# Kernel optimization log

Measured on AMD Instinct MI355X. Metric: run time of the kernel, lower is better.

The kernel has to match this reference:

```python
import jax, jax.numpy as jnp
import numpy as np

B, T, H, I = 256, 1024, 512, 1


def _uniform(key, shape, bound):
    return jax.random.uniform(key, shape, jnp.float32, -bound, bound)


def setup_inputs() -> dict:
    key = jax.random.key(0)
    ks = jax.random.split(key, 11)
    s = 1.0 / np.sqrt(H)
    return {
        "input": jax.random.normal(ks[0], (B, T), jnp.float32),
        "W_ih1": _uniform(ks[1], (3 * H, I), s),
        "W_hh1": _uniform(ks[2], (3 * H, H), s),
        "b_ih1": _uniform(ks[3], (3 * H,), s),
        "b_hh1": _uniform(ks[4], (3 * H,), s),
        "W_ih2": _uniform(ks[5], (3 * H, H), s),
        "W_hh2": _uniform(ks[6], (3 * H, H), s),
        "b_ih2": _uniform(ks[7], (3 * H,), s),
        "b_hh2": _uniform(ks[8], (3 * H,), s),
        "W_out": _uniform(ks[9], (1, H), s),
        "b_out": _uniform(ks[10], (1,), s),
        "future": 0,
    }


def _gru_cell(x, h, W_ih, W_hh, b_ih, b_hh):
    # PyTorch nn.GRUCell: gates ordered (r, z, n)
    gi = x @ W_ih.T + b_ih          # [B, 3H]
    gh = h @ W_hh.T + b_hh          # [B, 3H]
    i_r, i_z, i_n = jnp.split(gi, 3, axis=-1)
    h_r, h_z, h_n = jnp.split(gh, 3, axis=-1)
    r = jax.nn.sigmoid(i_r + h_r)
    z = jax.nn.sigmoid(i_z + h_z)
    n = jnp.tanh(i_n + r * h_n)
    return (1.0 - z) * n + z * h


def _run(input, W_ih1, W_hh1, b_ih1, b_hh1, W_ih2, W_hh2, b_ih2, b_hh2, W_out, b_out, future):
    Bb = input.shape[0]
    h0 = jnp.zeros((Bb, H), input.dtype)

    def step(carry, x_t):  # x_t: [B]
        h1, h2 = carry
        h1 = _gru_cell(x_t[:, None], h1, W_ih1, W_hh1, b_ih1, b_hh1)
        h2 = _gru_cell(h1, h2, W_ih2, W_hh2, b_ih2, b_hh2)
        out = h2 @ W_out.T + b_out  # [B, 1]
        return (h1, h2), out[:, 0]

    (h1, h2), ys = jax.lax.scan(step, (h0, h0), input.T)  # ys: [T, B]
    outs = [ys.T]  # [B, T]
    out = ys[-1][:, None]
    for _ in range(future):
        (h1, h2), o = step((h1, h2), out[:, 0])
        out = o[:, None]
        outs.append(out)
    return jnp.concatenate(outs, axis=1) if future > 0 else outs[0]


def reference(input, W_ih1, W_hh1, b_ih1, b_hh1, W_ih2, W_hh2, b_ih2, b_hh2, W_out, b_out, future):
    return _run(input, W_ih1, W_hh1, b_ih1, b_hh1, W_ih2, W_hh2, b_ih2, b_hh2, W_out, b_out, future)
```

## Files before the change

### kernel.cpp

```cpp
#include <hip/hip_runtime.h>

#define NB 256
#define NT 512
#define TT 1024
#define HH 512
#define BATCH 256

using v8s   = __attribute__((ext_vector_type(8))) short;
using f32x4 = __attribute__((ext_vector_type(4))) float;

#define O_RZ2I 0
#define O_RZ2H 32768
#define O_NA   65536
#define O_RZ1  98304
#define O_NB   131072
#define O_WOUT 147456
#define O_ZERO 149504
#define LDS_BYTES 162064

#define SLOT_SH 524288

__device__ __forceinline__ float sigf(float v)   { return 1.f / (1.f + __expf(-v)); }
__device__ __forceinline__ float tanhf_(float v) { return 2.f / (1.f + __expf(-2.f * v)) - 1.f; }

__device__ __forceinline__ unsigned short bf16_rne(float f) {
    union { float f; unsigned u; } a; a.f = f;
    unsigned r = (a.u + 0x7fffu + ((a.u >> 16) & 1u)) >> 16;
    return (unsigned short)r;
}
__device__ __forceinline__ float bf16_f(unsigned short h) {
    union { unsigned u; float f; } a; a.u = ((unsigned)h) << 16; return a.f;
}
__device__ __forceinline__ f32x4 MF(v8s a, v8s b, f32x4 c) {
    return __builtin_amdgcn_mfma_f32_16x16x32_bf16(a, b, c, 0, 0, 0);
}

#define GST2(addr, val) \
    asm volatile("global_store_short %0, %1, off sc0 sc1" \
                 :: "v"(addr), "v"(val) : "memory");

__device__ __forceinline__ void gridbar(unsigned* barr, int bg, int tid,
                                        unsigned ep, bool fence) {
    asm volatile("s_waitcnt vmcnt(0)" ::: "memory");
    __syncthreads();
    if (tid == 0) {
        unsigned* cnt = barr + bg * 64;
        __hip_atomic_fetch_add(cnt, 1u, __ATOMIC_RELAXED, __HIP_MEMORY_SCOPE_AGENT);
        while (__hip_atomic_load(cnt, __ATOMIC_RELAXED, __HIP_MEMORY_SCOPE_AGENT) < ep * 64u)
            __builtin_amdgcn_s_sleep(1);
        if (fence)
            __builtin_amdgcn_fence(__ATOMIC_ACQUIRE, "agent");
    }
    __syncthreads();
}

__global__ __launch_bounds__(256) void k_transpose(const float* __restrict__ x,
                                                   float* __restrict__ xT) {
    __shared__ float tile[64][65];
    const int bt = blockIdx.x, bb = blockIdx.y;
    const int lt = threadIdx.x & 63, lb = threadIdx.x >> 6;
    #pragma unroll 4
    for (int i = 0; i < 16; ++i) {
        int row = lb + i * 4;
        tile[row][lt] = x[(size_t)(bb * 64 + row) * TT + bt * 64 + lt];
    }
    __syncthreads();
    #pragma unroll 4
    for (int i = 0; i < 16; ++i) {
        int row = lb + i * 4;
        xT[(size_t)(bt * 64 + row) * BATCH + bb * 64 + lt] = tile[lt][row];
    }
}

__global__ __launch_bounds__(NT, 1) void gru_mfma(
    const float* __restrict__ xT,
    const float* __restrict__ Wih1, const float* __restrict__ Whh1,
    const float* __restrict__ bih1, const float* __restrict__ bhh1,
    const float* __restrict__ Wih2, const float* __restrict__ Whh2,
    const float* __restrict__ bih2, const float* __restrict__ bhh2,
    const float* __restrict__ Wout, const float* __restrict__ bout,
    float* __restrict__ out,
    unsigned short* __restrict__ hws,
    unsigned* __restrict__ barr,
    int rmask, int invmask)
{
    extern __shared__ char lds_b[];
    const int tid = threadIdx.x, blk = blockIdx.x;
    const int bg = blk >> 6, ug = blk & 63;
    const int u0 = ug * 8;

    for (int i = tid; i < 16 * 512; i += NT) {
        int n = i >> 9, k = i & 511;
        int row = (n < 8) ? (u0 + n) : (HH + u0 + (n - 8));
        float f = Wih2[(size_t)row * HH + k];
        unsigned short hi = bf16_rne(f), lo = bf16_rne(f - bf16_f(hi));
        int s = k >> 5, g = (k >> 3) & 3, j = k & 7, ln = g * 16 + n;
        int base = O_RZ2I + s * 2048 + ln * 16 + j * 2;
        *(unsigned short*)(lds_b + base) = hi;
        *(unsigned short*)(lds_b + base + 1024) = lo;
    }
    for (int i = tid; i < 16 * 512; i += NT) {
        int n = i >> 9, k = i & 511;
        int row = (n < 8) ? (u0 + n) : (HH + u0 + (n - 8));
        float f = Whh2[(size_t)row * HH + k];
        unsigned short hi = bf16_rne(f), lo = bf16_rne(f - bf16_f(hi));
        int s = k >> 5, g = (k >> 3) & 3, j = k & 7, ln = g * 16 + n;
        int base = O_RZ2H + s * 2048 + ln * 16 + j * 2;
        *(unsigned short*)(lds_b + base) = hi;
        *(unsigned short*)(lds_b + base + 1024) = lo;
    }
    for (int i = tid; i < 16 * 512; i += NT) {
        int n = i >> 9, k = i & 511;
        float f = (n < 8) ? Wih2[(size_t)(2 * HH + u0 + n) * HH + k]
                          : Whh1[(size_t)(2 * HH + u0 + (n - 8)) * HH + k];
        unsigned short hi = bf16_rne(f), lo = bf16_rne(f - bf16_f(hi));
        int s = k >> 5, g = (k >> 3) & 3, j = k & 7, ln = g * 16 + n;
        int base = O_NA + s * 2048 + ln * 16 + j * 2;
        *(unsigned short*)(lds_b + base) = hi;
        *(unsigned short*)(lds_b + base + 1024) = lo;
    }
    for (int i = tid; i < 16 * 512; i += NT) {
        int n = i >> 9, k = i & 511;
        int row = (n < 8) ? (u0 + n) : (HH + u0 + (n - 8));
        float f = Whh1[(size_t)row * HH + k];
        unsigned short hi = bf16_rne(f), lo = bf16_rne(f - bf16_f(hi));
        int s = k >> 5, g = (k >> 3) & 3, j = k & 7, ln = g * 16 + n;
        int base = O_RZ1 + s * 2048 + ln * 16 + j * 2;
        *(unsigned short*)(lds_b + base) = hi;
        *(unsigned short*)(lds_b + base + 1024) = lo;
    }
    for (int i = tid; i < 8 * 512; i += NT) {
        int c = i >> 9, k = i & 511;
        float f = Whh2[(size_t)(2 * HH + u0 + c) * HH + k];
        unsigned short hi = bf16_rne(f), lo = bf16_rne(f - bf16_f(hi));
        int s = k >> 5, g = (k >> 3) & 3, j = k & 7;
        int base = O_NB + s * 1024 + (g * 8 + c) * 16 + j * 2;
        *(unsigned short*)(lds_b + base) = hi;
        *(unsigned short*)(lds_b + base + 512) = lo;
    }
    for (int k = tid; k < 512; k += NT) {
        float f = Wout[k];
        unsigned short hi = bf16_rne(f), lo = bf16_rne(f - bf16_f(hi));
        int s = k >> 5, g = (k >> 3) & 3, j = k & 7;
        int base = O_WOUT + s * 64 + g * 16 + j * 2;
        *(unsigned short*)(lds_b + base) = hi;
        *(unsigned short*)(lds_b + base + 1024) = lo;
    }
    if (tid < 4) ((unsigned*)(lds_b + O_ZERO))[tid] = 0;

    {
        const int rl = tid >> 3, uo = tid & 7;
        const int b = bg * 64 + rl, u = u0 + uo;
        unsigned short* s0 = hws;
        GST2(s0 + 262144 + (size_t)b * HH + u, 0u);
        GST2(s0 + 393216 + (size_t)b * HH + u, 0u);
        float x0 = xT[b];
        float r = sigf(x0 * Wih1[u] + bih1[u] + bhh1[u]);
        float z = sigf(x0 * Wih1[HH + u] + bih1[HH + u] + bhh1[HH + u]);
        float n = tanhf_(x0 * Wih1[2 * HH + u] + bih1[2 * HH + u] + r * bhh1[2 * HH + u]);
        float h = (1.f - z) * n;
        unsigned short hi = bf16_rne(h), lo = bf16_rne(h - bf16_f(hi));
        GST2(s0 + (size_t)b * HH + u, (unsigned)hi);
        GST2(s0 + 131072 + (size_t)b * HH + u, (unsigned)lo);
    }

    const int w = tid >> 6, lane = tid & 63;
    const int n16 = lane & 15, g4 = lane >> 4;
    const int rt = w & 3, kh = w >> 2;
    const int c = n16, cu = c & 7;
    const int u = u0 + cu;
    const int sbase = kh * 8;

    float b2rz = 0, wx1 = 0, b1rz = 0, bin2_ = 0, bhn2_ = 0, wxn1 = 0, bin1_ = 0, bhn1_ = 0;
    float hprev[4] = {0.f, 0.f, 0.f, 0.f};
    if (kh == 1) {
        b2rz = (c < 8) ? bih2[u] + bhh2[u] : bih2[HH + u] + bhh2[HH + u];
        wx1  = (c < 8) ? Wih1[u] : Wih1[HH + u];
        b1rz = (c < 8) ? bih1[u] + bhh1[u] : bih1[HH + u] + bhh1[HH + u];
        bin2_ = bih2[2 * HH + u]; bhn2_ = bhh2[2 * HH + u];
        wxn1 = Wih1[2 * HH + u]; bin1_ = bih1[2 * HH + u]; bhn1_ = bhh1[2 * HH + u];
        if (c >= 8) {
            #pragma unroll
            for (int j = 0; j < 4; ++j) {
                int b = bg * 64 + rt * 16 + g4 * 4 + j;
                float x0 = xT[b];
                float r = sigf(x0 * Wih1[u] + bih1[u] + bhh1[u]);
                float z = sigf(x0 * Wih1[HH + u] + bih1[HH + u] + bhh1[HH + u]);
                float nn = tanhf_(x0 * Wih1[2 * HH + u] + bih1[2 * HH + u] + r * bhh1[2 * HH + u]);
                hprev[j] = (1.f - z) * nn;
            }
        }
    }
    const float boutv = bout[0];

    const char* BA = lds_b + O_NA   + lane * 16;
    const char* B1 = lds_b + O_RZ1  + lane * 16;
    const char* BBh = (n16 < 8) ? lds_b + O_NB + kh * 8192 + (g4 * 8 + n16) * 16
                                : lds_b + O_ZERO;
    const char* BBl = (n16 < 8) ? BBh + 512 : lds_b + O_ZERO;
    const int  bbs  = (n16 < 8) ? 1024 : 0;
    const char* Bo  = (n16 == 0) ? lds_b + O_WOUT + kh * 512 + g4 * 16 : lds_b + O_ZERO;
    const char* Bol = (n16 == 0) ? Bo + 1024 : lds_b + O_ZERO;
    const int  bos  = (n16 == 0) ? 64 : 0;

    float* scr = (float*)(lds_b + 0);
    float* so  = (float*)(lds_b + 32768);

    unsigned ep = 1;
    gridbar(barr, bg, tid, ep, true);

    v8s RBi[8][2], RBh[8][2];
    {
        const char* Bi = lds_b + O_RZ2I + lane * 16;
        const char* Bh = lds_b + O_RZ2H + lane * 16;
        #pragma unroll
        for (int s8 = 0; s8 < 8; ++s8) {
            const int s = sbase + s8;
            RBi[s8][0] = *(const v8s*)(Bi + s * 2048);
            RBi[s8][1] = *(const v8s*)(Bi + s * 2048 + 1024);
            RBh[s8][0] = *(const v8s*)(Bh + s * 2048);
            RBh[s8][1] = *(const v8s*)(Bh + s * 2048 + 1024);
        }
    }
    __syncthreads();

    for (int t = 0; t <= TT; ++t) {
        const unsigned short* __restrict__ slotR = hws + (size_t)(t & rmask) * SLOT_SH;
        unsigned short* __restrict__ slotW = hws + (size_t)((t + 1) & rmask) * SLOT_SH;
        const unsigned short* __restrict__ h1rh = slotR;
        const unsigned short* __restrict__ h1rl = slotR + 131072;
        const unsigned short* __restrict__ h2rh = slotR + 262144;
        const unsigned short* __restrict__ h2rl = slotR + 393216;
        unsigned short* h1wh = slotW;
        unsigned short* h1wl = slotW + 131072;
        unsigned short* h2wh = slotW + 262144;
        unsigned short* h2wl = slotW + 393216;

        const size_t aoff = ((size_t)(bg * 64 + rt * 16 + n16) * HH + (size_t)kh * 256 + g4 * 8);
        const unsigned short* __restrict__ pa1h = h1rh + aoff;
        const unsigned short* __restrict__ pa1l = h1rl + aoff;
        const unsigned short* __restrict__ pa2h = h2rh + aoff;
        const unsigned short* __restrict__ pa2l = h2rl + aoff;

        f32x4 ai = {0.f,0.f,0.f,0.f}, ah = {0.f,0.f,0.f,0.f}, a1v = {0.f,0.f,0.f,0.f};
        f32x4 aA = {0.f,0.f,0.f,0.f}, aB = {0.f,0.f,0.f,0.f}, ao = {0.f,0.f,0.f,0.f};

        #pragma unroll
        for (int sl = 0; sl < 8; ++sl) {
            const int s = sbase + sl;
            const v8s a1h = *(const v8s*)(pa1h + sl * 32);
            const v8s a1l = *(const v8s*)(pa1l + sl * 32);
            const v8s a2h = *(const v8s*)(pa2h + sl * 32);
            const v8s a2l = *(const v8s*)(pa2l + sl * 32);
            ai = MF(a1h, RBi[sl][0], ai); ai = MF(a1l, RBi[sl][0], ai); ai = MF(a1h, RBi[sl][1], ai);
            ah = MF(a2h, RBh[sl][0], ah); ah = MF(a2l, RBh[sl][0], ah); ah = MF(a2h, RBh[sl][1], ah);
            v8s bh, bl;
            bh = *(const v8s*)(BA + s * 2048); bl = *(const v8s*)(BA + s * 2048 + 1024);
            aA = MF(a1h, bh, aA); aA = MF(a1l, bh, aA); aA = MF(a1h, bl, aA);
            bh = *(const v8s*)(B1 + s * 2048); bl = *(const v8s*)(B1 + s * 2048 + 1024);
            a1v = MF(a1h, bh, a1v); a1v = MF(a1l, bh, a1v); a1v = MF(a1h, bl, a1v);
            bh = *(const v8s*)(BBh + sl * bbs); bl = *(const v8s*)(BBl + sl * bbs);
            aB = MF(a2h, bh, aB); aB = MF(a2l, bh, aB); aB = MF(a2h, bl, aB);
            bh = *(const v8s*)(Bo + sl * bos); bl = *(const v8s*)(Bol + sl * bos);
            ao = MF(a2h, bh, ao); ao = MF(a2l, bh, ao); ao = MF(a2h, bl, ao);
        }

        if (kh == 0) {
            #pragma unroll
            for (int j = 0; j < 4; ++j) {
                const int row = g4 * 4 + j;
                scr[(0 * 4 + rt) * 320 + row * 20 + c] = ai[j] + ah[j];
                scr[(1 * 4 + rt) * 320 + row * 20 + c] = a1v[j];
                scr[(2 * 4 + rt) * 320 + row * 20 + c] = aA[j];
                scr[(3 * 4 + rt) * 320 + row * 20 + c] = aB[j];
            }
            if (c == 0) {
                #pragma unroll
                for (int j = 0; j < 4; ++j) so[rt * 16 + g4 * 4 + j] = ao[j];
            }
        }
        __syncthreads();

        if (kh == 1) {
            float s2v[4], zz2[4], s1v[4], rr1[4], AAv[4], ABv[4], xvv[4];
            #pragma unroll
            for (int j = 0; j < 4; ++j) {
                const int row = g4 * 4 + j;
                const int b = bg * 64 + rt * 16 + row;
                const float AIAH = ai[j] + ah[j] + scr[(0 * 4 + rt) * 320 + row * 20 + c];
                const float A1v  = a1v[j] + scr[(1 * 4 + rt) * 320 + row * 20 + c];
                AAv[j] = aA[j] + scr[(2 * 4 + rt) * 320 + row * 20 + c];
                ABv[j] = aB[j] + scr[(3 * 4 + rt) * 320 + row * 20 + c];
                xvv[j] = (t + 1 < TT) ? xT[(size_t)(t + 1) * BATCH + b] : 0.f;
                s2v[j] = sigf(AIAH + b2rz);
                s1v[j] = sigf(xvv[j] * wx1 + b1rz + A1v);
            }
            #pragma unroll
            for (int j = 0; j < 4; ++j) {
                zz2[j] = __shfl_xor(s2v[j], 8);
                rr1[j] = __shfl_xor(s1v[j], 8);
            }
            #pragma unroll
            for (int j = 0; j < 4; ++j) {
                const int row = g4 * 4 + j;
                const int b = bg * 64 + rt * 16 + row;
                if (c < 8) {
                    if (t < TT) {
                        float n2 = tanhf_(AAv[j] + bin2_ + s2v[j] * (ABv[j] + bhn2_));
                        float hn = (1.f - zz2[j]) * n2 + zz2[j] * hprev[j];
                        hprev[j] = hn;
                        unsigned short hi = bf16_rne(hn), lo = bf16_rne(hn - bf16_f(hi));
                        GST2(h2wh + (size_t)b * HH + u, (unsigned)hi);
                        GST2(h2wl + (size_t)b * HH + u, (unsigned)lo);
                    }
                } else {
                    if (t + 1 < TT) {
                        float n1 = tanhf_(xvv[j] * wxn1 + bin1_ + rr1[j] * (AAv[j] + bhn1_));
                        float hn = (1.f - s1v[j]) * n1 + s1v[j] * hprev[j];
                        hprev[j] = hn;
                        unsigned short hi = bf16_rne(hn), lo = bf16_rne(hn - bf16_f(hi));
                        GST2(h1wh + (size_t)b * HH + u, (unsigned)hi);
                        GST2(h1wl + (size_t)b * HH + u, (unsigned)lo);
                    }
                }
                if (c == 0 && ug == 0 && t >= 1) {
                    float AO = ao[j] + so[rt * 16 + row];
                    out[(size_t)b * TT + (t - 1)] = AO + boutv;
                }
            }
        }
        ++ep;
        gridbar(barr, bg, tid, ep, (t & invmask) == invmask);
    }
}

extern "C" void kernel_launch(void* const* d_in, const int* in_sizes, int n_in,
                              void* d_out, int out_size, void* d_ws, size_t ws_size,
                              hipStream_t stream) {
    const float* x    = (const float*)d_in[0];
    const float* Wih1 = (const float*)d_in[1];
    const float* Whh1 = (const float*)d_in[2];
    const float* bih1 = (const float*)d_in[3];
    const float* bhh1 = (const float*)d_in[4];
    const float* Wih2 = (const float*)d_in[5];
    const float* Whh2 = (const float*)d_in[6];
    const float* bih2 = (const float*)d_in[7];
    const float* bhh2 = (const float*)d_in[8];
    const float* Wout = (const float*)d_in[9];
    const float* bout = (const float*)d_in[10];
    float* outp = (float*)d_out;

    const size_t MB = 1048576;
    size_t avail = (ws_size > MB + 8192) ? ws_size - MB - 8192 : 2 * MB;
    int R = 2;
    while (R < 64 && (size_t)(R * 2) * MB <= avail) R *= 2;
    const int INVP = (R >= 4) ? (R / 2) : 1;

    unsigned short* hws = (unsigned short*)d_ws;
    float* xT      = (float*)((char*)d_ws + (size_t)R * MB);
    unsigned* barr = (unsigned*)((char*)d_ws + (size_t)R * MB + MB);

    hipMemsetAsync((void*)barr, 0, 8192, stream);
    k_transpose<<<dim3(16, 4), 256, 0, stream>>>(x, xT);

    hipFuncSetAttribute((const void*)gru_mfma,
                        hipFuncAttributeMaxDynamicSharedMemorySize, LDS_BYTES);

    int rmask = R - 1, invmask = INVP - 1;
    void* args[] = { (void*)&xT,
                     (void*)&Wih1, (void*)&Whh1, (void*)&bih1, (void*)&bhh1,
                     (void*)&Wih2, (void*)&Whh2, (void*)&bih2, (void*)&bhh2,
                     (void*)&Wout, (void*)&bout,
                     (void*)&outp, (void*)&hws, (void*)&barr,
                     (void*)&rmask, (void*)&invmask };
    hipLaunchCooperativeKernel((void*)gru_mfma, dim3(NB), dim3(NT),
                               args, LDS_BYTES, stream);
}
```

Before: 11.07 ms.

## Repartition GRU blocks to 32 batch rows by 16 units with per-gate warp groups

Each block now covers 32 batch rows by 16 hidden units instead of 64 by 8, so the grid splits into 8 batch groups of 32 blocks. The per-group barrier now waits on 32 arrivals instead of 64. Warps are split into four gate-specialised groups that hold their weight tiles in registers and publish partial sums to LDS, after which every thread runs the elementwise update for one (batch, unit) element. The hidden-state workspace is also laid out per batch group. This is meant to cut barrier participants and spread the MFMA work more evenly, at the cost of an LDS reduction round per step and higher register pressure.

```diff
diff --git a/kernel.cpp b/kernel.cpp
--- a/kernel.cpp
+++ b/kernel.cpp
@@ -5,18 +5,19 @@
 #define TT 1024
 #define HH 512
 #define BATCH 256
+#define UB 16
+#define BGB 32
 
 using v8s   = __attribute__((ext_vector_type(8))) short;
 using f32x4 = __attribute__((ext_vector_type(4))) float;
 
-#define O_RZ2I 0
-#define O_RZ2H 32768
-#define O_NA   65536
-#define O_RZ1  98304
-#define O_NB   131072
-#define O_WOUT 147456
-#define O_ZERO 149504
-#define LDS_BYTES 162064
+#define O_STG  0
+#define O_N1   32768
+#define O_WOUT 65536
+#define O_ZERO 67584
+#define O_SCR  67600
+#define O_SO   113680
+#define LDS_BYTES 113936
 
 #define SLOT_SH 524288
 
@@ -34,10 +35,12 @@
 __device__ __forceinline__ f32x4 MF(v8s a, v8s b, f32x4 c) {
     return __builtin_amdgcn_mfma_f32_16x16x32_bf16(a, b, c, 0, 0, 0);
 }
+#define T3(ACC, AH_, AL_, BH_, BL_) \
+    ACC = MF(AH_, BH_, ACC); ACC = MF(AL_, BH_, ACC); ACC = MF(AH_, BL_, ACC);
 
 #define GST2(addr, val) \
     asm volatile("global_store_short %0, %1, off sc0 sc1" \
-                 :: "v"(addr), "v"(val) : "memory");
+                 :: "v"(addr), "v"((unsigned)(val)) : "memory");
 
 __device__ __forceinline__ void gridbar(unsigned* barr, int bg, int tid,
                                         unsigned ep, bool fence) {
@@ -46,7 +49,7 @@
     if (tid == 0) {
         unsigned* cnt = barr + bg * 64;
         __hip_atomic_fetch_add(cnt, 1u, __ATOMIC_RELAXED, __HIP_MEMORY_SCOPE_AGENT);
-        while (__hip_atomic_load(cnt, __ATOMIC_RELAXED, __HIP_MEMORY_SCOPE_AGENT) < ep * 64u)
+        while (__hip_atomic_load(cnt, __ATOMIC_RELAXED, __HIP_MEMORY_SCOPE_AGENT) < ep * 32u)
             __builtin_amdgcn_s_sleep(1);
         if (fence)
             __builtin_amdgcn_fence(__ATOMIC_ACQUIRE, "agent");
@@ -71,6 +74,27 @@
         xT[(size_t)(bt * 64 + row) * BATCH + bb * 64 + lt] = tile[lt][row];
     }
 }
+
+#define STAGE_TILE(SRC) \
+    for (int i = tid; i < 16 * 512; i += NT) { \
+        int n = i >> 9, k = i & 511; \
+        float f = (SRC)[(size_t)(u0 + n) * HH + k]; \
+        unsigned short hi = bf16_rne(f), lo = bf16_rne(f - bf16_f(hi)); \
+        int s = k >> 5, g = (k >> 3) & 3, j = k & 7, ln = g * 16 + n; \
+        int base = O_STG + s * 2048 + ln * 16 + j * 2; \
+        *(unsigned short*)(lds_b + base) = hi; \
+        *(unsigned short*)(lds_b + base + 1024) = lo; }
+
+#define GRAB(RB) { \
+    const char* bp = lds_b + O_STG + lane * 16; \
+    _Pragma("unroll") for (int s8 = 0; s8 < 8; ++s8) { \
+        RB[s8][0] = *(const v8s*)(bp + (kh * 8 + s8) * 2048); \
+        RB[s8][1] = *(const v8s*)(bp + (kh * 8 + s8) * 2048 + 1024); } }
+
+#define PUB(TAU, A0, A1v) \
+    _Pragma("unroll") for (int j = 0; j < 4; ++j) { \
+        sk[(TAU) * 640 + (g4 * 4 + j) * 20 + n16]      = (A0)[j]; \
+        sk[(TAU) * 640 + (16 + g4 * 4 + j) * 20 + n16] = (A1v)[j]; }
 
 __global__ __launch_bounds__(NT, 1) void gru_mfma(
     const float* __restrict__ xT,
@@ -86,57 +110,35 @@
 {
     extern __shared__ char lds_b[];
     const int tid = threadIdx.x, blk = blockIdx.x;
-    const int bg = blk >> 6, ug = blk & 63;
-    const int u0 = ug * 8;
-
+
+    const int bg   = blk >> 5;
+    const int slot = blk & 31;
+    const int u0   = slot * UB;
+    const bool doOut = (slot == 0);
+
+    const int w = tid >> 6, lane = tid & 63;
+    const int n16 = lane & 15, g4 = lane >> 4;
+    const int kh = w & 1, tg = w >> 1;
+
+    if (tid < 4) ((unsigned*)(lds_b + O_ZERO))[tid] = 0;
+    v8s RB0[8][2], RB1[8][2];
+    const size_t G = (size_t)HH * HH;
+    STAGE_TILE(Whh2)          __syncthreads(); if (tg == 0) GRAB(RB0) __syncthreads();
+    STAGE_TILE(Whh2 + G)      __syncthreads(); if (tg == 0) GRAB(RB1) __syncthreads();
+    STAGE_TILE(Wih2)          __syncthreads(); if (tg == 1) GRAB(RB0) __syncthreads();
+    STAGE_TILE(Wih2 + G)      __syncthreads(); if (tg == 1) GRAB(RB1) __syncthreads();
+    STAGE_TILE(Wih2 + 2 * G)  __syncthreads(); if (tg == 2) GRAB(RB0) __syncthreads();
+    STAGE_TILE(Whh2 + 2 * G)  __syncthreads(); if (tg == 2) GRAB(RB1) __syncthreads();
+    STAGE_TILE(Whh1)          __syncthreads(); if (tg == 3) GRAB(RB0) __syncthreads();
+    STAGE_TILE(Whh1 + G)      __syncthreads(); if (tg == 3) GRAB(RB1) __syncthreads();
     for (int i = tid; i < 16 * 512; i += NT) {
         int n = i >> 9, k = i & 511;
-        int row = (n < 8) ? (u0 + n) : (HH + u0 + (n - 8));
-        float f = Wih2[(size_t)row * HH + k];
+        float f = Whh1[2 * G + (size_t)(u0 + n) * HH + k];
         unsigned short hi = bf16_rne(f), lo = bf16_rne(f - bf16_f(hi));
         int s = k >> 5, g = (k >> 3) & 3, j = k & 7, ln = g * 16 + n;
-        int base = O_RZ2I + s * 2048 + ln * 16 + j * 2;
+        int base = O_N1 + s * 2048 + ln * 16 + j * 2;
         *(unsigned short*)(lds_b + base) = hi;
         *(unsigned short*)(lds_b + base + 1024) = lo;
-    }
-    for (int i = tid; i < 16 * 512; i += NT) {
-        int n = i >> 9, k = i & 511;
-        int row = (n < 8) ? (u0 + n) : (HH + u0 + (n - 8));
-        float f = Whh2[(size_t)row * HH + k];
-        unsigned short hi = bf16_rne(f), lo = bf16_rne(f - bf16_f(hi));
-        int s = k >> 5, g = (k >> 3) & 3, j = k & 7, ln = g * 16 + n;
-        int base = O_RZ2H + s * 2048 + ln * 16 + j * 2;
-        *(unsigned short*)(lds_b + base) = hi;
-        *(unsigned short*)(lds_b + base + 1024) = lo;
-    }
-    for (int i = tid; i < 16 * 512; i += NT) {
-        int n = i >> 9, k = i & 511;
-        float f = (n < 8) ? Wih2[(size_t)(2 * HH + u0 + n) * HH + k]
-                          : Whh1[(size_t)(2 * HH + u0 + (n - 8)) * HH + k];
-        unsigned short hi = bf16_rne(f), lo = bf16_rne(f - bf16_f(hi));
-        int s = k >> 5, g = (k >> 3) & 3, j = k & 7, ln = g * 16 + n;
-        int base = O_NA + s * 2048 + ln * 16 + j * 2;
-        *(unsigned short*)(lds_b + base) = hi;
-        *(unsigned short*)(lds_b + base + 1024) = lo;
-    }
-    for (int i = tid; i < 16 * 512; i += NT) {
-        int n = i >> 9, k = i & 511;
-        int row = (n < 8) ? (u0 + n) : (HH + u0 + (n - 8));
-        float f = Whh1[(size_t)row * HH + k];
-        unsigned short hi = bf16_rne(f), lo = bf16_rne(f - bf16_f(hi));
-        int s = k >> 5, g = (k >> 3) & 3, j = k & 7, ln = g * 16 + n;
-        int base = O_RZ1 + s * 2048 + ln * 16 + j * 2;
-        *(unsigned short*)(lds_b + base) = hi;
-        *(unsigned short*)(lds_b + base + 1024) = lo;
-    }
-    for (int i = tid; i < 8 * 512; i += NT) {
-        int c = i >> 9, k = i & 511;
-        float f = Whh2[(size_t)(2 * HH + u0 + c) * HH + k];
-        unsigned short hi = bf16_rne(f), lo = bf16_rne(f - bf16_f(hi));
-        int s = k >> 5, g = (k >> 3) & 3, j = k & 7;
-        int base = O_NB + s * 1024 + (g * 8 + c) * 16 + j * 2;
-        *(unsigned short*)(lds_b + base) = hi;
-        *(unsigned short*)(lds_b + base + 512) = lo;
     }
     for (int k = tid; k < 512; k += NT) {
         float f = Wout[k];
@@ -146,187 +148,189 @@
         *(unsigned short*)(lds_b + base) = hi;
         *(unsigned short*)(lds_b + base + 1024) = lo;
     }
-    if (tid < 4) ((unsigned*)(lds_b + O_ZERO))[tid] = 0;
-
+
+    const int u = tid & 15, b = tid >> 4;
+    const int gu = u0 + u;
+    const int gb = bg * BGB + b;
+    const float b2r  = bih2[gu] + bhh2[gu];
+    const float b2z  = bih2[HH + gu] + bhh2[HH + gu];
+    const float b2in = bih2[2 * HH + gu], b2hn = bhh2[2 * HH + gu];
+    const float w1r = Wih1[gu], w1z = Wih1[HH + gu], w1n = Wih1[2 * HH + gu];
+    const float b1r = bih1[gu] + bhh1[gu];
+    const float b1z = bih1[HH + gu] + bhh1[HH + gu];
+    const float b1ni = bih1[2 * HH + gu], b1nh = bhh1[2 * HH + gu];
+    const float bo = bout[0];
+
+    float h1prev, h2prev = 0.f;
     {
-        const int rl = tid >> 3, uo = tid & 7;
-        const int b = bg * 64 + rl, u = u0 + uo;
-        unsigned short* s0 = hws;
-        GST2(s0 + 262144 + (size_t)b * HH + u, 0u);
-        GST2(s0 + 393216 + (size_t)b * HH + u, 0u);
-        float x0 = xT[b];
-        float r = sigf(x0 * Wih1[u] + bih1[u] + bhh1[u]);
-        float z = sigf(x0 * Wih1[HH + u] + bih1[HH + u] + bhh1[HH + u]);
-        float n = tanhf_(x0 * Wih1[2 * HH + u] + bih1[2 * HH + u] + r * bhh1[2 * HH + u]);
-        float h = (1.f - z) * n;
-        unsigned short hi = bf16_rne(h), lo = bf16_rne(h - bf16_f(hi));
-        GST2(s0 + (size_t)b * HH + u, (unsigned)hi);
-        GST2(s0 + 131072 + (size_t)b * HH + u, (unsigned)lo);
-    }
-
-    const int w = tid >> 6, lane = tid & 63;
-    const int n16 = lane & 15, g4 = lane >> 4;
-    const int rt = w & 3, kh = w >> 2;
-    const int c = n16, cu = c & 7;
-    const int u = u0 + cu;
-    const int sbase = kh * 8;
-
-    float b2rz = 0, wx1 = 0, b1rz = 0, bin2_ = 0, bhn2_ = 0, wxn1 = 0, bin1_ = 0, bhn1_ = 0;
-    float hprev[4] = {0.f, 0.f, 0.f, 0.f};
-    if (kh == 1) {
-        b2rz = (c < 8) ? bih2[u] + bhh2[u] : bih2[HH + u] + bhh2[HH + u];
-        wx1  = (c < 8) ? Wih1[u] : Wih1[HH + u];
-        b1rz = (c < 8) ? bih1[u] + bhh1[u] : bih1[HH + u] + bhh1[HH + u];
-        bin2_ = bih2[2 * HH + u]; bhn2_ = bhh2[2 * HH + u];
-        wxn1 = Wih1[2 * HH + u]; bin1_ = bih1[2 * HH + u]; bhn1_ = bhh1[2 * HH + u];
-        if (c >= 8) {
-            #pragma unroll
-            for (int j = 0; j < 4; ++j) {
-                int b = bg * 64 + rt * 16 + g4 * 4 + j;
-                float x0 = xT[b];
-                float r = sigf(x0 * Wih1[u] + bih1[u] + bhh1[u]);
-                float z = sigf(x0 * Wih1[HH + u] + bih1[HH + u] + bhh1[HH + u]);
-                float nn = tanhf_(x0 * Wih1[2 * HH + u] + bih1[2 * HH + u] + r * bhh1[2 * HH + u]);
-                hprev[j] = (1.f - z) * nn;
-            }
-        }
-    }
-    const float boutv = bout[0];
-
-    const char* BA = lds_b + O_NA   + lane * 16;
-    const char* B1 = lds_b + O_RZ1  + lane * 16;
-    const char* BBh = (n16 < 8) ? lds_b + O_NB + kh * 8192 + (g4 * 8 + n16) * 16
-                                : lds_b + O_ZERO;
-    const char* BBl = (n16 < 8) ? BBh + 512 : lds_b + O_ZERO;
-    const int  bbs  = (n16 < 8) ? 1024 : 0;
-    const char* Bo  = (n16 == 0) ? lds_b + O_WOUT + kh * 512 + g4 * 16 : lds_b + O_ZERO;
-    const char* Bol = (n16 == 0) ? Bo + 1024 : lds_b + O_ZERO;
-    const int  bos  = (n16 == 0) ? 64 : 0;
-
-    float* scr = (float*)(lds_b + 0);
-    float* so  = (float*)(lds_b + 32768);
+        unsigned short* s0 = hws + (size_t)bg * 65536;
+        float x0 = xT[gb];
+        float r = sigf(x0 * w1r + b1r);
+        float z = sigf(x0 * w1z + b1z);
+        float n = tanhf_(x0 * w1n + b1ni + r * b1nh);
+        h1prev = (1.f - z) * n;
+        unsigned short hi = bf16_rne(h1prev), lo = bf16_rne(h1prev - bf16_f(hi));
+        GST2(s0 + (size_t)b * 512 + gu, hi);
+        GST2(s0 + 16384 + (size_t)b * 512 + gu, lo);
+        GST2(s0 + 32768 + (size_t)b * 512 + gu, 0u);
+        GST2(s0 + 49152 + (size_t)b * 512 + gu, 0u);
+    }
+
+    const char* n1p  = lds_b + O_N1 + lane * 16;
+    const char* BoP  = (n16 == 0) ? lds_b + O_WOUT + kh * 512 + g4 * 16
+                                  : lds_b + O_ZERO;
+    const char* BolP = (n16 == 0) ? BoP + 1024 : lds_b + O_ZERO;
+    const int bos = (n16 == 0) ? 64 : 0;
+    float* sk = (float*)(lds_b + O_SCR) + kh * 5760;
+
+    const int rowA = n16 * 512 + kh * 256 + g4 * 8;
 
     unsigned ep = 1;
     gridbar(barr, bg, tid, ep, true);
 
-    v8s RBi[8][2], RBh[8][2];
-    {
-        const char* Bi = lds_b + O_RZ2I + lane * 16;
-        const char* Bh = lds_b + O_RZ2H + lane * 16;
+    for (int t = 0; t <= TT; ++t) {
+        const unsigned short* __restrict__ setR =
+            hws + (size_t)(t & rmask) * SLOT_SH + (size_t)bg * 65536;
+        unsigned short* __restrict__ setW =
+            hws + (size_t)((t + 1) & rmask) * SLOT_SH + (size_t)bg * 65536;
+
+        const unsigned short* __restrict__ p1h0 = setR + rowA;
+        const unsigned short* __restrict__ p1h1 = p1h0 + 8192;
+        const unsigned short* __restrict__ p1l0 = setR + 16384 + rowA;
+        const unsigned short* __restrict__ p1l1 = p1l0 + 8192;
+        const unsigned short* __restrict__ p2h0 = setR + 32768 + rowA;
+        const unsigned short* __restrict__ p2h1 = p2h0 + 8192;
+        const unsigned short* __restrict__ p2l0 = setR + 49152 + rowA;
+        const unsigned short* __restrict__ p2l1 = p2l0 + 8192;
+
+        f32x4 acc[2][2];
         #pragma unroll
-        for (int s8 = 0; s8 < 8; ++s8) {
-            const int s = sbase + s8;
-            RBi[s8][0] = *(const v8s*)(Bi + s * 2048);
-            RBi[s8][1] = *(const v8s*)(Bi + s * 2048 + 1024);
-            RBh[s8][0] = *(const v8s*)(Bh + s * 2048);
-            RBh[s8][1] = *(const v8s*)(Bh + s * 2048 + 1024);
-        }
-    }
-    __syncthreads();
-
-    for (int t = 0; t <= TT; ++t) {
-        const unsigned short* __restrict__ slotR = hws + (size_t)(t & rmask) * SLOT_SH;
-        unsigned short* __restrict__ slotW = hws + (size_t)((t + 1) & rmask) * SLOT_SH;
-        const unsigned short* __restrict__ h1rh = slotR;
-        const unsigned short* __restrict__ h1rl = slotR + 131072;
-        const unsigned short* __restrict__ h2rh = slotR + 262144;
-        const unsigned short* __restrict__ h2rl = slotR + 393216;
-        unsigned short* h1wh = slotW;
-        unsigned short* h1wl = slotW + 131072;
-        unsigned short* h2wh = slotW + 262144;
-        unsigned short* h2wl = slotW + 393216;
-
-        const size_t aoff = ((size_t)(bg * 64 + rt * 16 + n16) * HH + (size_t)kh * 256 + g4 * 8);
-        const unsigned short* __restrict__ pa1h = h1rh + aoff;
-        const unsigned short* __restrict__ pa1l = h1rl + aoff;
-        const unsigned short* __restrict__ pa2h = h2rh + aoff;
-        const unsigned short* __restrict__ pa2l = h2rl + aoff;
-
-        f32x4 ai = {0.f,0.f,0.f,0.f}, ah = {0.f,0.f,0.f,0.f}, a1v = {0.f,0.f,0.f,0.f};
-        f32x4 aA = {0.f,0.f,0.f,0.f}, aB = {0.f,0.f,0.f,0.f}, ao = {0.f,0.f,0.f,0.f};
-
-        #pragma unroll
-        for (int sl = 0; sl < 8; ++sl) {
-            const int s = sbase + sl;
-            const v8s a1h = *(const v8s*)(pa1h + sl * 32);
-            const v8s a1l = *(const v8s*)(pa1l + sl * 32);
-            const v8s a2h = *(const v8s*)(pa2h + sl * 32);
-            const v8s a2l = *(const v8s*)(pa2l + sl * 32);
-            ai = MF(a1h, RBi[sl][0], ai); ai = MF(a1l, RBi[sl][0], ai); ai = MF(a1h, RBi[sl][1], ai);
-            ah = MF(a2h, RBh[sl][0], ah); ah = MF(a2l, RBh[sl][0], ah); ah = MF(a2h, RBh[sl][1], ah);
-            v8s bh, bl;
-            bh = *(const v8s*)(BA + s * 2048); bl = *(const v8s*)(BA + s * 2048 + 1024);
-            aA = MF(a1h, bh, aA); aA = MF(a1l, bh, aA); aA = MF(a1h, bl, aA);
-            bh = *(const v8s*)(B1 + s * 2048); bl = *(const v8s*)(B1 + s * 2048 + 1024);
-            a1v = MF(a1h, bh, a1v); a1v = MF(a1l, bh, a1v); a1v = MF(a1h, bl, a1v);
-            bh = *(const v8s*)(BBh + sl * bbs); bl = *(const v8s*)(BBl + sl * bbs);
-            aB = MF(a2h, bh, aB); aB = MF(a2l, bh, aB); aB = MF(a2h, bl, aB);
-            bh = *(const v8s*)(Bo + sl * bos); bl = *(const v8s*)(Bol + sl * bos);
-            ao = MF(a2h, bh, ao); ao = MF(a2l, bh, ao); ao = MF(a2h, bl, ao);
-        }
-
-        if (kh == 0) {
-            #pragma unroll
-            for (int j = 0; j < 4; ++j) {
-                const int row = g4 * 4 + j;
-                scr[(0 * 4 + rt) * 320 + row * 20 + c] = ai[j] + ah[j];
-                scr[(1 * 4 + rt) * 320 + row * 20 + c] = a1v[j];
-                scr[(2 * 4 + rt) * 320 + row * 20 + c] = aA[j];
-                scr[(3 * 4 + rt) * 320 + row * 20 + c] = aB[j];
-            }
-            if (c == 0) {
+        for (int m = 0; m < 2; ++m)
+            #pragma unroll
+            for (int q = 0; q < 2; ++q) acc[m][q] = (f32x4){0.f, 0.f, 0.f, 0.f};
+        f32x4 ao[2] = {{0.f,0.f,0.f,0.f}, {0.f,0.f,0.f,0.f}};
+
+        if (tg == 0) {
+            #pragma unroll
+            for (int sl = 0; sl < 8; ++sl) {
+                const v8s a0h = *(const v8s*)(p2h0 + sl * 32);
+                const v8s a0l = *(const v8s*)(p2l0 + sl * 32);
+                const v8s a1h = *(const v8s*)(p2h1 + sl * 32);
+                const v8s a1l = *(const v8s*)(p2l1 + sl * 32);
+                T3(acc[0][0], a0h, a0l, RB0[sl][0], RB0[sl][1])
+                T3(acc[1][0], a1h, a1l, RB0[sl][0], RB0[sl][1])
+                T3(acc[0][1], a0h, a0l, RB1[sl][0], RB1[sl][1])
+                T3(acc[1][1], a1h, a1l, RB1[sl][0], RB1[sl][1])
+                if (doOut) {
+                    v8s wh = *(const v8s*)(BoP + sl * bos);
+                    v8s wl = *(const v8s*)(BolP + sl * bos);
+                    T3(ao[0], a0h, a0l, wh, wl)
+                    T3(ao[1], a1h, a1l, wh, wl)
+                }
+            }
+            PUB(3, acc[0][0], acc[1][0])
+            PUB(4, acc[0][1], acc[1][1])
+            if (doOut && n16 == 0) {
+                float* sp = (float*)(lds_b + O_SO) + kh * 32;
                 #pragma unroll
-                for (int j = 0; j < 4; ++j) so[rt * 16 + g4 * 4 + j] = ao[j];
-            }
+                for (int j = 0; j < 4; ++j) {
+                    sp[g4 * 4 + j]      = ao[0][j];
+                    sp[16 + g4 * 4 + j] = ao[1][j];
+                }
+            }
+        } else if (tg == 1) {
+            #pragma unroll
+            for (int sl = 0; sl < 8; ++sl) {
+                const v8s a0h = *(const v8s*)(p1h0 + sl * 32);
+                const v8s a0l = *(const v8s*)(p1l0 + sl * 32);
+                const v8s a1h = *(const v8s*)(p1h1 + sl * 32);
+                const v8s a1l = *(const v8s*)(p1l1 + sl * 32);
+                T3(acc[0][0], a0h, a0l, RB0[sl][0], RB0[sl][1])
+                T3(acc[1][0], a1h, a1l, RB0[sl][0], RB0[sl][1])
+                T3(acc[0][1], a0h, a0l, RB1[sl][0], RB1[sl][1])
+                T3(acc[1][1], a1h, a1l, RB1[sl][0], RB1[sl][1])
+            }
+            PUB(0, acc[0][0], acc[1][0])
+            PUB(1, acc[0][1], acc[1][1])
+        } else if (tg == 2) {
+            #pragma unroll
+            for (int sl = 0; sl < 8; ++sl) {
+                const v8s a0h = *(const v8s*)(p1h0 + sl * 32);
+                const v8s a0l = *(const v8s*)(p1l0 + sl * 32);
+                const v8s a1h = *(const v8s*)(p1h1 + sl * 32);
+                const v8s a1l = *(const v8s*)(p1l1 + sl * 32);
+                T3(acc[0][0], a0h, a0l, RB0[sl][0], RB0[sl][1])
+                T3(acc[1][0], a1h, a1l, RB0[sl][0], RB0[sl][1])
+                const v8s c0h = *(const v8s*)(p2h0 + sl * 32);
+                const v8s c0l = *(const v8s*)(p2l0 + sl * 32);
+                const v8s c1h = *(const v8s*)(p2h1 + sl * 32);
+                const v8s c1l = *(const v8s*)(p2l1 + sl * 32);
+                T3(acc[0][1], c0h, c0l, RB1[sl][0], RB1[sl][1])
+                T3(acc[1][1], c1h, c1l, RB1[sl][0], RB1[sl][1])
+            }
+            PUB(2, acc[0][0], acc[1][0])
+            PUB(5, acc[0][1], acc[1][1])
+        } else {
+            f32x4 an[2] = {{0.f,0.f,0.f,0.f}, {0.f,0.f,0.f,0.f}};
+            #pragma unroll
+            for (int sl = 0; sl < 8; ++sl) {
+                const v8s a0h = *(const v8s*)(p1h0 + sl * 32);
+                const v8s a0l = *(const v8s*)(p1l0 + sl * 32);
+                const v8s a1h = *(const v8s*)(p1h1 + sl * 32);
+                const v8s a1l = *(const v8s*)(p1l1 + sl * 32);
+                T3(acc[0][0], a0h, a0l, RB0[sl][0], RB0[sl][1])
+                T3(acc[1][0], a1h, a1l, RB0[sl][0], RB0[sl][1])
+                T3(acc[0][1], a0h, a0l, RB1[sl][0], RB1[sl][1])
+                T3(acc[1][1], a1h, a1l, RB1[sl][0], RB1[sl][1])
+                const v8s nh = *(const v8s*)(n1p + (kh * 8 + sl) * 2048);
+                const v8s nl = *(const v8s*)(n1p + (kh * 8 + sl) * 2048 + 1024);
+                T3(an[0], a0h, a0l, nh, nl)
+                T3(an[1], a1h, a1l, nh, nl)
+            }
+            PUB(6, acc[0][0], acc[1][0])
+            PUB(7, acc[0][1], acc[1][1])
+            PUB(8, an[0], an[1])
         }
         __syncthreads();
 
-        if (kh == 1) {
-            float s2v[4], zz2[4], s1v[4], rr1[4], AAv[4], ABv[4], xvv[4];
-            #pragma unroll
-            for (int j = 0; j < 4; ++j) {
-                const int row = g4 * 4 + j;
-                const int b = bg * 64 + rt * 16 + row;
-                const float AIAH = ai[j] + ah[j] + scr[(0 * 4 + rt) * 320 + row * 20 + c];
-                const float A1v  = a1v[j] + scr[(1 * 4 + rt) * 320 + row * 20 + c];
-                AAv[j] = aA[j] + scr[(2 * 4 + rt) * 320 + row * 20 + c];
-                ABv[j] = aB[j] + scr[(3 * 4 + rt) * 320 + row * 20 + c];
-                xvv[j] = (t + 1 < TT) ? xT[(size_t)(t + 1) * BATCH + b] : 0.f;
-                s2v[j] = sigf(AIAH + b2rz);
-                s1v[j] = sigf(xvv[j] * wx1 + b1rz + A1v);
-            }
-            #pragma unroll
-            for (int j = 0; j < 4; ++j) {
-                zz2[j] = __shfl_xor(s2v[j], 8);
-                rr1[j] = __shfl_xor(s1v[j], 8);
-            }
-            #pragma unroll
-            for (int j = 0; j < 4; ++j) {
-                const int row = g4 * 4 + j;
-                const int b = bg * 64 + rt * 16 + row;
-                if (c < 8) {
-                    if (t < TT) {
-                        float n2 = tanhf_(AAv[j] + bin2_ + s2v[j] * (ABv[j] + bhn2_));
-                        float hn = (1.f - zz2[j]) * n2 + zz2[j] * hprev[j];
-                        hprev[j] = hn;
-                        unsigned short hi = bf16_rne(hn), lo = bf16_rne(hn - bf16_f(hi));
-                        GST2(h2wh + (size_t)b * HH + u, (unsigned)hi);
-                        GST2(h2wl + (size_t)b * HH + u, (unsigned)lo);
-                    }
-                } else {
-                    if (t + 1 < TT) {
-                        float n1 = tanhf_(xvv[j] * wxn1 + bin1_ + rr1[j] * (AAv[j] + bhn1_));
-                        float hn = (1.f - s1v[j]) * n1 + s1v[j] * hprev[j];
-                        hprev[j] = hn;
-                        unsigned short hi = bf16_rne(hn), lo = bf16_rne(hn - bf16_f(hi));
-                        GST2(h1wh + (size_t)b * HH + u, (unsigned)hi);
-                        GST2(h1wl + (size_t)b * HH + u, (unsigned)lo);
-                    }
-                }
-                if (c == 0 && ug == 0 && t >= 1) {
-                    float AO = ao[j] + so[rt * 16 + row];
-                    out[(size_t)b * TT + (t - 1)] = AO + boutv;
-                }
+        {
+            const float* sA = (const float*)(lds_b + O_SCR);
+            const float* sB = sA + 5760;
+            const int ei = b * 20 + u;
+            float v0 = sA[0 * 640 + ei] + sB[0 * 640 + ei];
+            float v1 = sA[1 * 640 + ei] + sB[1 * 640 + ei];
+            float v2 = sA[2 * 640 + ei] + sB[2 * 640 + ei];
+            float v3 = sA[3 * 640 + ei] + sB[3 * 640 + ei];
+            float v4 = sA[4 * 640 + ei] + sB[4 * 640 + ei];
+            float v5 = sA[5 * 640 + ei] + sB[5 * 640 + ei];
+            float v6 = sA[6 * 640 + ei] + sB[6 * 640 + ei];
+            float v7 = sA[7 * 640 + ei] + sB[7 * 640 + ei];
+            float v8 = sA[8 * 640 + ei] + sB[8 * 640 + ei];
+
+            float r2 = sigf(v0 + v3 + b2r);
+            float z2 = sigf(v1 + v4 + b2z);
+            float n2 = tanhf_(v2 + b2in + r2 * (v5 + b2hn));
+            float h2n = (1.f - z2) * n2 + z2 * h2prev;
+            if (t < TT) {
+                h2prev = h2n;
+                unsigned short hi = bf16_rne(h2n), lo = bf16_rne(h2n - bf16_f(hi));
+                GST2(setW + 32768 + (size_t)b * 512 + gu, hi);
+                GST2(setW + 49152 + (size_t)b * 512 + gu, lo);
+            }
+            float xv = (t + 1 < TT) ? xT[(size_t)(t + 1) * BATCH + gb] : 0.f;
+            float r1 = sigf(xv * w1r + v6 + b1r);
+            float z1 = sigf(xv * w1z + v7 + b1z);
+            float n1 = tanhf_(xv * w1n + b1ni + r1 * (v8 + b1nh));
+            float h1n = (1.f - z1) * n1 + z1 * h1prev;
+            if (t + 1 < TT) {
+                h1prev = h1n;
+                unsigned short hi = bf16_rne(h1n), lo = bf16_rne(h1n - bf16_f(hi));
+                GST2(setW + (size_t)b * 512 + gu, hi);
+                GST2(setW + 16384 + (size_t)b * 512 + gu, lo);
+            }
+            if (doOut && u == 0 && t >= 1) {
+                const float* sp = (const float*)(lds_b + O_SO);
+                out[(size_t)gb * TT + (t - 1)] = sp[b] + sp[32 + b] + bo;
             }
         }
         ++ep;
@@ -357,17 +361,17 @@
     const int INVP = (R >= 4) ? (R / 2) : 1;
 
     unsigned short* hws = (unsigned short*)d_ws;
-    float* xT      = (float*)((char*)d_ws + (size_t)R * MB);
+    float* xTp     = (float*)((char*)d_ws + (size_t)R * MB);
     unsigned* barr = (unsigned*)((char*)d_ws + (size_t)R * MB + MB);
 
     hipMemsetAsync((void*)barr, 0, 8192, stream);
-    k_transpose<<<dim3(16, 4), 256, 0, stream>>>(x, xT);
+    k_transpose<<<dim3(16, 4), 256, 0, stream>>>(x, xTp);
 
     hipFuncSetAttribute((const void*)gru_mfma,
                         hipFuncAttributeMaxDynamicSharedMemorySize, LDS_BYTES);
 
     int rmask = R - 1, invmask = INVP - 1;
-    void* args[] = { (void*)&xT,
+    void* args[] = { (void*)&xTp,
                      (void*)&Wih1, (void*)&Whh1, (void*)&bih1, (void*)&bhh1,
                      (void*)&Wih2, (void*)&Whh2, (void*)&bih2, (void*)&bhh2,
                      (void*)&Wout, (void*)&bout,
```

Result: slower. 12.22 ms (+10.4%).

## Use plain stores with release barrier, interleave block mapping, prefetch x early

Applied to the files above, without the earlier changes.

Replaces the inline-asm system-coherent (sc0 sc1) global stores with ordinary stores and makes the barrier arrival atomic a release operation so the hidden-state writes are published through the atomic. Block-to-group mapping is interleaved (bg = blk & 3), which changes how the blocks of each batch group are spread across the device. The next-step input load is hoisted ahead of the MFMA loop so its latency is hidden behind the matmul. This risks coherence problems if the release semantics do not flush the plain stores to where other CUs read them.

```diff
diff --git a/kernel.cpp b/kernel.cpp
--- a/kernel.cpp
+++ b/kernel.cpp
@@ -35,17 +35,13 @@
     return __builtin_amdgcn_mfma_f32_16x16x32_bf16(a, b, c, 0, 0, 0);
 }
 
-#define GST2(addr, val) \
-    asm volatile("global_store_short %0, %1, off sc0 sc1" \
-                 :: "v"(addr), "v"(val) : "memory");
-
 __device__ __forceinline__ void gridbar(unsigned* barr, int bg, int tid,
                                         unsigned ep, bool fence) {
     asm volatile("s_waitcnt vmcnt(0)" ::: "memory");
     __syncthreads();
     if (tid == 0) {
         unsigned* cnt = barr + bg * 64;
-        __hip_atomic_fetch_add(cnt, 1u, __ATOMIC_RELAXED, __HIP_MEMORY_SCOPE_AGENT);
+        __hip_atomic_fetch_add(cnt, 1u, __ATOMIC_RELEASE, __HIP_MEMORY_SCOPE_AGENT);
         while (__hip_atomic_load(cnt, __ATOMIC_RELAXED, __HIP_MEMORY_SCOPE_AGENT) < ep * 64u)
             __builtin_amdgcn_s_sleep(1);
         if (fence)
@@ -86,7 +82,7 @@
 {
     extern __shared__ char lds_b[];
     const int tid = threadIdx.x, blk = blockIdx.x;
-    const int bg = blk >> 6, ug = blk & 63;
+    const int bg = blk & 3, ug = blk >> 2;
     const int u0 = ug * 8;
 
     for (int i = tid; i < 16 * 512; i += NT) {
@@ -152,16 +148,16 @@
         const int rl = tid >> 3, uo = tid & 7;
         const int b = bg * 64 + rl, u = u0 + uo;
         unsigned short* s0 = hws;
-        GST2(s0 + 262144 + (size_t)b * HH + u, 0u);
-        GST2(s0 + 393216 + (size_t)b * HH + u, 0u);
+        s0[262144 + (size_t)b * HH + u] = 0;
+        s0[393216 + (size_t)b * HH + u] = 0;
         float x0 = xT[b];
         float r = sigf(x0 * Wih1[u] + bih1[u] + bhh1[u]);
         float z = sigf(x0 * Wih1[HH + u] + bih1[HH + u] + bhh1[HH + u]);
         float n = tanhf_(x0 * Wih1[2 * HH + u] + bih1[2 * HH + u] + r * bhh1[2 * HH + u]);
         float h = (1.f - z) * n;
         unsigned short hi = bf16_rne(h), lo = bf16_rne(h - bf16_f(hi));
-        GST2(s0 + (size_t)b * HH + u, (unsigned)hi);
-        GST2(s0 + 131072 + (size_t)b * HH + u, (unsigned)lo);
+        s0[(size_t)b * HH + u] = hi;
+        s0[131072 + (size_t)b * HH + u] = lo;
     }
 
     const int w = tid >> 6, lane = tid & 63;
@@ -241,6 +237,13 @@
         const unsigned short* __restrict__ pa1l = h1rl + aoff;
         const unsigned short* __restrict__ pa2h = h2rh + aoff;
         const unsigned short* __restrict__ pa2l = h2rl + aoff;
+
+        float xpre[4];
+        #pragma unroll
+        for (int j = 0; j < 4; ++j) {
+            const int brow = bg * 64 + rt * 16 + g4 * 4 + j;
+            xpre[j] = (t + 1 < TT) ? xT[(size_t)(t + 1) * BATCH + brow] : 0.f;
+        }
 
         f32x4 ai = {0.f,0.f,0.f,0.f}, ah = {0.f,0.f,0.f,0.f}, a1v = {0.f,0.f,0.f,0.f};
         f32x4 aA = {0.f,0.f,0.f,0.f}, aB = {0.f,0.f,0.f,0.f}, ao = {0.f,0.f,0.f,0.f};
@@ -282,18 +285,16 @@
         __syncthreads();
 
         if (kh == 1) {
-            float s2v[4], zz2[4], s1v[4], rr1[4], AAv[4], ABv[4], xvv[4];
+            float s2v[4], zz2[4], s1v[4], rr1[4], AAv[4], ABv[4];
             #pragma unroll
             for (int j = 0; j < 4; ++j) {
                 const int row = g4 * 4 + j;
-                const int b = bg * 64 + rt * 16 + row;
                 const float AIAH = ai[j] + ah[j] + scr[(0 * 4 + rt) * 320 + row * 20 + c];
                 const float A1v  = a1v[j] + scr[(1 * 4 + rt) * 320 + row * 20 + c];
                 AAv[j] = aA[j] + scr[(2 * 4 + rt) * 320 + row * 20 + c];
                 ABv[j] = aB[j] + scr[(3 * 4 + rt) * 320 + row * 20 + c];
-                xvv[j] = (t + 1 < TT) ? xT[(size_t)(t + 1) * BATCH + b] : 0.f;
                 s2v[j] = sigf(AIAH + b2rz);
-                s1v[j] = sigf(xvv[j] * wx1 + b1rz + A1v);
+                s1v[j] = sigf(xpre[j] * wx1 + b1rz + A1v);
             }
             #pragma unroll
             for (int j = 0; j < 4; ++j) {
@@ -310,17 +311,17 @@
                         float hn = (1.f - zz2[j]) * n2 + zz2[j] * hprev[j];
                         hprev[j] = hn;
                         unsigned short hi = bf16_rne(hn), lo = bf16_rne(hn - bf16_f(hi));
-                        GST2(h2wh + (size_t)b * HH + u, (unsigned)hi);
-                        GST2(h2wl + (size_t)b * HH + u, (unsigned)lo);
+                        h2wh[(size_t)b * HH + u] = hi;
+                        h2wl[(size_t)b * HH + u] = lo;
                     }
                 } else {
                     if (t + 1 < TT) {
-                        float n1 = tanhf_(xvv[j] * wxn1 + bin1_ + rr1[j] * (AAv[j] + bhn1_));
+                        float n1 = tanhf_(xpre[j] * wxn1 + bin1_ + rr1[j] * (AAv[j] + bhn1_));
                         float hn = (1.f - s1v[j]) * n1 + s1v[j] * hprev[j];
                         hprev[j] = hn;
                         unsigned short hi = bf16_rne(hn), lo = bf16_rne(hn - bf16_f(hi));
-                        GST2(h1wh + (size_t)b * HH + u, (unsigned)hi);
-                        GST2(h1wl + (size_t)b * HH + u, (unsigned)lo);
+                        h1wh[(size_t)b * HH + u] = hi;
+                        h1wl[(size_t)b * HH + u] = lo;
                     }
                 }
                 if (c == 0 && ug == 0 && t >= 1) {
@@ -357,17 +358,17 @@
     const int INVP = (R >= 4) ? (R / 2) : 1;
 
     unsigned short* hws = (unsigned short*)d_ws;
-    float* xT      = (float*)((char*)d_ws + (size_t)R * MB);
+    float* xTp     = (float*)((char*)d_ws + (size_t)R * MB);
     unsigned* barr = (unsigned*)((char*)d_ws + (size_t)R * MB + MB);
 
     hipMemsetAsync((void*)barr, 0, 8192, stream);
-    k_transpose<<<dim3(16, 4), 256, 0, stream>>>(x, xT);
+    k_transpose<<<dim3(16, 4), 256, 0, stream>>>(x, xTp);
 
     hipFuncSetAttribute((const void*)gru_mfma,
                         hipFuncAttributeMaxDynamicSharedMemorySize, LDS_BYTES);
 
     int rmask = R - 1, invmask = INVP - 1;
-    void* args[] = { (void*)&xT,
+    void* args[] = { (void*)&xTp,
                      (void*)&Wih1, (void*)&Whh1, (void*)&bih1, (void*)&bhh1,
                      (void*)&Wih2, (void*)&Whh2, (void*)&bih2, (void*)&bhh2,
                      (void*)&Wout, (void*)&bout,
```

Result: slower. 15.63 ms (+41.2%).
